# Performance work log

Measured on AMD Instinct MI355X. Metric: run time of the kernel, lower is better.

Reference implementation:

```python
import jax, jax.numpy as jnp
import numpy as np

WIN = (6, 6, 6)
HEADS = 4
DIM = 96
SPATIAL = (48, 48, 48)


def _window_partition(x, ws):
    # x: (b, d, h, w, c) -> (num_windows*b, wd*wh*ww, c)
    b, d, h, w, c = x.shape
    wd, wh, ww = ws
    x = x.reshape(b, d // wd, wd, h // wh, wh, w // ww, ww, c)
    x = x.transpose(0, 1, 3, 5, 2, 4, 6, 7)
    return x.reshape(-1, wd * wh * ww, c)


def _window_reverse(win, ws, b, d, h, w, c):
    wd, wh, ww = ws
    x = win.reshape(b, d // wd, h // wh, w // ww, wd, wh, ww, c)
    x = x.transpose(0, 1, 4, 2, 5, 3, 6, 7)
    return x.reshape(b, d, h, w, c)


def _rel_index(ws):
    # static numpy computation of relative-position index table, (n, n) int
    wd, wh, ww = ws
    coords = np.stack(np.meshgrid(np.arange(wd), np.arange(wh), np.arange(ww), indexing='ij'))
    cf = coords.reshape(3, -1)
    rc = (cf[:, :, None] - cf[:, None, :]).transpose(1, 2, 0).astype(np.int64)
    rc[..., 0] += wd - 1
    rc[..., 1] += wh - 1
    rc[..., 2] += ww - 1
    rc[..., 0] *= (2 * wh - 1) * (2 * ww - 1)
    rc[..., 1] *= (2 * ww - 1)
    return rc.sum(-1)


def _shift_mask(d, h, w, ws, ss):
    # static numpy mask, (nW, n, n) float32 with 0 / -100
    wd, wh, ww = ws
    sd, sh, sw = ss
    m = np.zeros((1, d, h, w, 1), np.float32)
    cnt = 0
    for dsl in (slice(0, -wd), slice(-wd, -sd), slice(-sd, None)):
        for hsl in (slice(0, -wh), slice(-wh, -sh), slice(-sh, None)):
            for wsl in (slice(0, -ww), slice(-ww, -sw), slice(-sw, None)):
                m[:, dsl, hsl, wsl, :] = cnt
                cnt += 1
    mw = m.reshape(1, d // wd, wd, h // wh, wh, w // ww, ww, 1)
    mw = mw.transpose(0, 1, 3, 5, 2, 4, 6, 7).reshape(-1, wd * wh * ww)
    am = mw[:, None, :] - mw[:, :, None]
    return np.where(am != 0, np.float32(-100.0), np.float32(0.0))


def _conv1x1(x, W, b):
    # 1x1x1 Conv3d == channel matmul; x: (b,c,d,h,w), W: (out,in)
    return jnp.einsum('bcdhw,oc->bodhw', x, W) + b[None, :, None, None, None]


def setup_inputs() -> dict:
    key = jax.random.key(0)
    ks = jax.random.split(key, 12)
    shp = (1, DIM) + SPATIAL
    table_size = (2 * WIN[0] - 1) * (2 * WIN[1] - 1) * (2 * WIN[2] - 1)
    s = 1.0 / np.sqrt(DIM)
    return {
        'q_in': jax.random.normal(ks[0], shp, jnp.float32),
        'k_in': jax.random.normal(ks[1], shp, jnp.float32),
        'v_in': jax.random.normal(ks[2], shp, jnp.float32),
        'Wq': jax.random.normal(ks[3], (DIM, DIM), jnp.float32) * s,
        'bq': jnp.zeros((DIM,), jnp.float32),
        'Wk': jax.random.normal(ks[4], (DIM, DIM), jnp.float32) * s,
        'bk': jnp.zeros((DIM,), jnp.float32),
        'Wv': jax.random.normal(ks[5], (DIM, DIM), jnp.float32) * s,
        'bv': jnp.zeros((DIM,), jnp.float32),
        'Wp': jax.random.normal(ks[6], (DIM, DIM), jnp.float32) * s,
        'bp': jnp.zeros((DIM,), jnp.float32),
        'rel_table': jax.random.normal(ks[7], (table_size, HEADS), jnp.float32) * 0.02,
        'use_shift': 1,
    }


def reference(q_in, k_in, v_in, Wq, bq, Wk, bk, Wv, bv, Wp, bp, rel_table, use_shift):
    b, c, d, h, w = q_in.shape
    wd, wh, ww = WIN
    hd = DIM // HEADS
    scale = hd ** -0.5
    shift = bool(use_shift)
    ss = (wd // 2, wh // 2, ww // 2) if shift else (0, 0, 0)

    q = _conv1x1(q_in, Wq, bq)
    k = _conv1x1(k_in, Wk, bk)
    v = _conv1x1(v_in, Wv, bv)
    # d,h,w divisible by window -> no padding needed
    if shift:
        q = jnp.roll(q, (-ss[0], -ss[1], -ss[2]), axis=(2, 3, 4))
        k = jnp.roll(k, (-ss[0], -ss[1], -ss[2]), axis=(2, 3, 4))
        v = jnp.roll(v, (-ss[0], -ss[1], -ss[2]), axis=(2, 3, 4))

    qw = _window_partition(q.transpose(0, 2, 3, 4, 1), WIN)
    kw = _window_partition(k.transpose(0, 2, 3, 4, 1), WIN)
    vw = _window_partition(v.transpose(0, 2, 3, 4, 1), WIN)
    nw, n, _ = qw.shape
    qw = qw.reshape(nw, n, HEADS, hd).transpose(0, 2, 1, 3)
    kw = kw.reshape(nw, n, HEADS, hd).transpose(0, 2, 1, 3)
    vw = vw.reshape(nw, n, HEADS, hd).transpose(0, 2, 1, 3)

    attn = jnp.einsum('whnd,whmd->whnm', qw * scale, kw)  # (nw, H, n, n)
    idx = _rel_index(WIN)
    bias = rel_table[idx.reshape(-1)].reshape(n, n, HEADS).transpose(2, 0, 1)
    attn = attn + bias[None]
    if shift:
        mask = jnp.asarray(_shift_mask(d, h, w, WIN, ss))  # (nW, n, n)
        nW = mask.shape[0]
        attn = attn.reshape(b, nW, HEADS, n, n) + mask[None, :, None]
        attn = attn.reshape(nw, HEADS, n, n)
    attn = jax.nn.softmax(attn, axis=-1)
    out = jnp.einsum('whnm,whmd->whnd', attn, vw)
    out = out.transpose(0, 2, 1, 3).reshape(nw, n, c)
    out = _window_reverse(out, WIN, b, d, h, w, c)
    if shift:
        out = jnp.roll(out, ss, axis=(1, 2, 3))
    out = out.transpose(0, 4, 1, 2, 3)
    out = _conv1x1(out, Wp, bp)
    return out
```

## Files before the change

### kernel.cpp

```cpp
#include <hip/hip_runtime.h>
#include <hip/hip_bf16.h>


#define CH    96
#define DS    48
#define NVOX  (48*48*48)
#define WSZ   6
#define NWIN  512
#define NTOK  216
#define NTOKP 224
#define NHEADS 4
#define HD    24
#define XSTR  100
#define VSTR  228
#define PGRID (NVOX / 128)
#define CEXP  8.0f

typedef __attribute__((ext_vector_type(4))) float  f32x4;
typedef __attribute__((ext_vector_type(4))) short  s16x4;
typedef __attribute__((ext_vector_type(8))) short  s16x8;
typedef __attribute__((ext_vector_type(8))) _Float16 f16x8;

static __device__ inline short f2b(float f) {
    union { float f; unsigned u; } v; v.f = f;
    unsigned r = v.u + 0x7FFF + ((v.u >> 16) & 1);
    return (short)(r >> 16);
}
static __device__ inline float bf2f(short s) {
    union { unsigned u; float f; } v;
    v.u = ((unsigned)(unsigned short)s) << 16;
    return v.f;
}
static __device__ inline unsigned pack_f16(float a, float b) {
    unsigned short ua = __builtin_bit_cast(unsigned short, (_Float16)a);
    unsigned short ub = __builtin_bit_cast(unsigned short, (_Float16)b);
    return (unsigned)ua | ((unsigned)ub << 16);
}

__global__ __launch_bounds__(256) void wconv_kernel(
    const float* __restrict__ W0, const float* __restrict__ W1,
    const float* __restrict__ W2, const float* __restrict__ W3,
    short* __restrict__ Wf)
{
    int idx = blockIdx.x * 256 + threadIdx.x;
    int m = idx / 9216;
    int r = idx - m * 9216;
    const float* W = (m == 0) ? W0 : ((m == 1) ? W1 : ((m == 2) ? W2 : W3));
    Wf[idx] = __builtin_bit_cast(short, (_Float16)W[r]);
}

__global__ __launch_bounds__(256) void eb_kernel(
    const float* __restrict__ rel_table, float* __restrict__ EB)
{
    int idx = blockIdx.x * 256 + threadIdx.x;
    int head = idx / (8 * NTOKP * NTOKP);
    int rem = idx - head * 8 * NTOKP * NTOKP;
    int ty = rem / (NTOKP * NTOKP);
    int rem2 = rem - ty * NTOKP * NTOKP;
    int i = rem2 / NTOKP;
    int j = rem2 - (rem2 / NTOKP) * NTOKP;
    float val = 0.f;
    if (i < NTOK && j < NTOK) {
        int tdi = i / 36, thi = (i / 6) % 6, twi = i % 6;
        int tdj = j / 36, thj = (j / 6) % 6, twj = j % 6;
        bool m = ((ty & 1) && ((tdi < 3) != (tdj < 3))) ||
                 ((ty & 2) && ((thi < 3) != (thj < 3))) ||
                 ((ty & 4) && ((twi < 3) != (twj < 3)));
        int ridx = ((tdi - tdj + 5) * 11 + (thi - thj + 5)) * 11 + (twi - twj + 5);
        float b = rel_table[ridx * NHEADS + head];
        val = m ? 0.f : __expf(b - CEXP);
    }
    EB[idx] = val;
}

__global__ __launch_bounds__(256) void proj_mfma_kernel(
    const float* __restrict__ x0, const float* __restrict__ x1, const float* __restrict__ x2,
    const short* __restrict__ Wf,
    const float* __restrict__ b0, const float* __restrict__ b1, const float* __restrict__ b2,
    const int* __restrict__ use_shift,
    short* __restrict__ d0, short* __restrict__ d1, short* __restrict__ d2,
    float scale0)
{
    __shared__ short Xs[128 * XSTR];

    int tid = threadIdx.x;
    int which = blockIdx.x / PGRID;
    int bx = blockIdx.x - which * PGRID;
    int v0 = bx * 128;

    const float* x    = (which == 0) ? x0 : ((which == 1) ? x1 : x2);
    const float* bias = (which == 0) ? b0 : ((which == 1) ? b1 : b2);
    short*       dst  = (which == 0) ? d0 : ((which == 1) ? d1 : d2);
    const short* Wfp  = Wf + which * 9216;
    float scale = (which == 0) ? scale0 : 1.0f;

    {
        int vox = tid & 127;
        int v = v0 + vox;
        int d = v / (DS * DS);
        int rem = v - d * DS * DS;
        int h = rem / DS;
        int w = rem - h * DS;
        int s = (use_shift[0] != 0) ? 3 : 0;
        int sd = d + s; if (sd >= DS) sd -= DS;
        int s_h = h + s; if (s_h >= DS) s_h -= DS;
        int s_w = w + s; if (s_w >= DS) s_w -= DS;
        int src = (sd * DS + s_h) * DS + s_w;
        for (int e = tid; e < 128 * 48; e += 256) {
            int kp = e >> 7;
            float xa = x[(2 * kp) * NVOX + src];
            float xb = x[(2 * kp + 1) * NVOX + src];
            *(unsigned*)&Xs[vox * XSTR + 2 * kp] = pack_f16(xa, xb);
        }
    }
    __syncthreads();

    const int wid = tid >> 6;
    const int lane = tid & 63;
    const int g = lane >> 4;
    const int c = lane & 15;
    const int mrow = wid * 32;

    const f32x4 zero4 = {0.f, 0.f, 0.f, 0.f};
    f32x4 acc[2][6];
#pragma unroll
    for (int i = 0; i < 2; i++)
#pragma unroll
        for (int j = 0; j < 6; j++) acc[i][j] = zero4;

#pragma unroll
    for (int kt = 0; kt < 3; kt++) {
        const short* pa0 = &Xs[(mrow + c) * XSTR + kt * 32 + g * 8];
        s16x4 a0l = *(const s16x4*)pa0;
        s16x4 a0h = *(const s16x4*)(pa0 + 4);
        f16x8 a0 = __builtin_bit_cast(f16x8,
            __builtin_shufflevector(a0l, a0h, 0, 1, 2, 3, 4, 5, 6, 7));
        const short* pa1 = &Xs[(mrow + 16 + c) * XSTR + kt * 32 + g * 8];
        s16x4 a1l = *(const s16x4*)pa1;
        s16x4 a1h = *(const s16x4*)(pa1 + 4);
        f16x8 a1 = __builtin_bit_cast(f16x8,
            __builtin_shufflevector(a1l, a1h, 0, 1, 2, 3, 4, 5, 6, 7));
#pragma unroll
        for (int nt = 0; nt < 6; nt++) {
            f16x8 bb = __builtin_bit_cast(f16x8,
                *(const s16x8*)&Wfp[(nt * 16 + c) * CH + kt * 32 + g * 8]);
            acc[0][nt] = __builtin_amdgcn_mfma_f32_16x16x32_f16(a0, bb, acc[0][nt], 0, 0, 0);
            acc[1][nt] = __builtin_amdgcn_mfma_f32_16x16x32_f16(a1, bb, acc[1][nt], 0, 0, 0);
        }
    }

    float bs[6];
#pragma unroll
    for (int nt = 0; nt < 6; nt++) bs[nt] = bias[nt * 16 + c];

    __syncthreads();

#pragma unroll
    for (int mtile = 0; mtile < 2; mtile++)
#pragma unroll
        for (int nt = 0; nt < 6; nt++)
#pragma unroll
            for (int r = 0; r < 4; r++) {
                int vox = mrow + mtile * 16 + g * 4 + r;
                int oc = nt * 16 + c;
                Xs[vox * XSTR + oc] = f2b((acc[mtile][nt][r] + bs[nt]) * scale);
            }
    __syncthreads();

    for (int e = tid; e < 512; e += 256) {
        int vox = e >> 2, q = e & 3;
        int v = v0 + vox;
        int d = v / (DS * DS);
        int rem = v - d * DS * DS;
        int h = rem / DS;
        int w = rem - h * DS;
        int widx = (d / WSZ) * 64 + (h / WSZ) * 8 + (w / WSZ);
        int tok  = (d % WSZ) * 36 + (h % WSZ) * WSZ + (w % WSZ);
        short* dp = dst + ((size_t)(widx * NHEADS + q) * NTOK + tok) * HD;
        const short* sp = &Xs[vox * XSTR + q * 24];
        s16x4 a0 = *(const s16x4*)(sp);
        s16x4 a1 = *(const s16x4*)(sp + 4);
        s16x4 a2 = *(const s16x4*)(sp + 8);
        s16x4 a3 = *(const s16x4*)(sp + 12);
        s16x4 a4 = *(const s16x4*)(sp + 16);
        s16x4 a5 = *(const s16x4*)(sp + 20);
        *(s16x8*)(dp)      = __builtin_shufflevector(a0, a1, 0, 1, 2, 3, 4, 5, 6, 7);
        *(s16x8*)(dp + 8)  = __builtin_shufflevector(a2, a3, 0, 1, 2, 3, 4, 5, 6, 7);
        *(s16x8*)(dp + 16) = __builtin_shufflevector(a4, a5, 0, 1, 2, 3, 4, 5, 6, 7);
    }
}

__global__ __launch_bounds__(256) void attn_mfma_kernel(
    const short* __restrict__ qw, const short* __restrict__ kw,
    const short* __restrict__ vw, const float* __restrict__ EB,
    const int* __restrict__ use_shift, short* __restrict__ aw)
{
    __shared__ short Ks[NTOK * 36];
    __shared__ short Vt[32 * VSTR];
    __shared__ short PO[4][576];

    int widx = blockIdx.x >> 2;
    int head = blockIdx.x & 3;
    int tid = threadIdx.x;
    bool shift = (use_shift[0] != 0);
    int wd = widx >> 6, wh = (widx >> 3) & 7, ww = widx & 7;
    int ty = shift ? ((wd == 7 ? 1 : 0) | (wh == 7 ? 2 : 0) | (ww == 7 ? 4 : 0)) : 0;

    {
        int* z2 = (int*)Ks; int* z3 = (int*)Vt;
        for (int i = tid; i < NTOK * 18; i += 256) z2[i] = 0;
        for (int i = tid; i < 16 * VSTR; i += 256)
            z3[i] = (i >= 12 * VSTR && i < (25 * VSTR) / 2) ? 0x3F803F80 : 0;
    }
    __syncthreads();

    const size_t hbase = (size_t)(widx * NHEADS + head) * NTOK * HD;

    for (int e = tid; e < NTOK * 3; e += 256) {
        int t = e / 3, ch = e - t * 3;
        const short* kp = kw + hbase + t * 24 + ch * 8;
        s16x8 k8 = *(const s16x8*)kp;
        *(s16x4*)&Ks[t * 36 + ch * 8]     = __builtin_shufflevector(k8, k8, 0, 1, 2, 3);
        *(s16x4*)&Ks[t * 36 + ch * 8 + 4] = __builtin_shufflevector(k8, k8, 4, 5, 6, 7);
        s16x8 v8 = *(const s16x8*)(vw + hbase + t * 24 + ch * 8);
#pragma unroll
        for (int j = 0; j < 8; j++) Vt[(ch * 8 + j) * VSTR + t] = v8[j];
    }
    __syncthreads();

    const int wid = tid >> 6;
    const int lane = tid & 63;
    const int g = lane >> 4;
    const int c = lane & 15;

    const f32x4 zero4 = {0.f, 0.f, 0.f, 0.f};
    short* myPs = &PO[wid][0];
    const float* EBt = EB + (size_t)(head * 8 + ty) * NTOKP * NTOKP;

    for (int mt = wid; mt < 14; mt += 4) {
        int m0 = mt * 16;
        s16x8 aq = {0, 0, 0, 0, 0, 0, 0, 0};
        int qtok = m0 + c;
        if (g < 3 && qtok < NTOK)
            aq = *(const s16x8*)(qw + hbase + (size_t)qtok * HD + g * 8);
        f32x4 sreg[14];
#pragma unroll
        for (int t = 0; t < 14; t++) {
            int krow = (t < 13) ? (t * 16 + c) : (208 + (c & 7));
            const short* p = &Ks[krow * 36 + g * 8];
            s16x4 lo = *(const s16x4*)p;
            s16x4 hi = *(const s16x4*)(p + 4);
            s16x8 bk = __builtin_shufflevector(lo, hi, 0, 1, 2, 3, 4, 5, 6, 7);
            sreg[t] = __builtin_amdgcn_mfma_f32_16x16x32_bf16(aq, bk, zero4, 0, 0, 0);
        }
        const float* ebr[4];
#pragma unroll
        for (int r = 0; r < 4; r++)
            ebr[r] = EBt + (size_t)(m0 + g * 4 + r) * NTOKP + c;
#pragma unroll
        for (int t = 0; t < 14; t++)
#pragma unroll
            for (int r = 0; r < 4; r++)
                sreg[t][r] = __expf(sreg[t][r]) * ebr[r][t * 16];

        f32x4 o0 = zero4, o1 = zero4;
#pragma unroll
        for (int kt = 0; kt < 7; kt++) {
#pragma unroll
            for (int tt = 0; tt < 2; tt++) {
                int t = kt * 2 + tt;
#pragma unroll
                for (int r = 0; r < 4; r++)
                    myPs[(g * 4 + r) * 36 + tt * 16 + c] = f2b(sreg[t][r]);
            }
            const short* p = &myPs[c * 36 + g * 8];
            s16x4 lo = *(const s16x4*)p;
            s16x4 hi = *(const s16x4*)(p + 4);
            s16x8 ap = __builtin_shufflevector(lo, hi, 0, 1, 2, 3, 4, 5, 6, 7);
            const short* pv0 = &Vt[c * VSTR + kt * 32 + g * 8];
            s16x4 v0l = *(const s16x4*)pv0;
            s16x4 v0h = *(const s16x4*)(pv0 + 4);
            s16x8 bv0 = __builtin_shufflevector(v0l, v0h, 0, 1, 2, 3, 4, 5, 6, 7);
            const short* pv1 = &Vt[(16 + c) * VSTR + kt * 32 + g * 8];
            s16x4 v1l = *(const s16x4*)pv1;
            s16x4 v1h = *(const s16x4*)(pv1 + 4);
            s16x8 bv1 = __builtin_shufflevector(v1l, v1h, 0, 1, 2, 3, 4, 5, 6, 7);
            o0 = __builtin_amdgcn_mfma_f32_16x16x32_bf16(ap, bv0, o0, 0, 0, 0);
            o1 = __builtin_amdgcn_mfma_f32_16x16x32_bf16(ap, bv1, o1, 0, 0, 0);
        }

#pragma unroll
        for (int r = 0; r < 4; r++) {
            float sm = __shfl(o1[r], (lane & 48) + 8);
            float ri = 1.f / sm;
            int row = g * 4 + r;
            myPs[row * 24 + c] = f2b(o0[r] * ri);
            if (c < 8) myPs[row * 24 + 16 + c] = f2b(o1[r] * ri);
        }
        int nrow = NTOK - m0; if (nrow > 16) nrow = 16;
        int nsh = nrow * 24;
        short* dstw = aw + hbase + (size_t)m0 * HD;
        for (int j = lane; j * 8 < nsh; j += 64)
            *(s16x8*)(dstw + j * 8) = *(const s16x8*)(myPs + j * 8);
    }
}

__global__ __launch_bounds__(256) void out_proj_mfma_kernel(
    const short* __restrict__ aw, const short* __restrict__ Wfp,
    const float* __restrict__ bp, const int* __restrict__ use_shift,
    float* __restrict__ out)
{
    __shared__ short Xs[128 * XSTR];

    int tid = threadIdx.x;
    int v0 = blockIdx.x * 128;

    for (int e = tid; e < 512; e += 256) {
        int vox = e >> 2, hq = e & 3;
        int v = v0 + vox;
        int d = v / (DS * DS);
        int rem = v - d * DS * DS;
        int h = rem / DS;
        int w = rem - h * DS;
        int s = (use_shift[0] != 0) ? 3 : 0;
        int sd = d - s; if (sd < 0) sd += DS;
        int s_h = h - s; if (s_h < 0) s_h += DS;
        int s_w = w - s; if (s_w < 0) s_w += DS;
        int widx = (sd / WSZ) * 64 + (s_h / WSZ) * 8 + (s_w / WSZ);
        int tok  = (sd % WSZ) * 36 + (s_h % WSZ) * WSZ + (s_w % WSZ);
        const short* sp = aw + ((size_t)(widx * NHEADS + hq) * NTOK + tok) * HD;
#pragma unroll
        for (int j3 = 0; j3 < 3; j3++) {
            s16x8 a = *(const s16x8*)(sp + 8 * j3);
#pragma unroll
            for (int p = 0; p < 4; p++)
                *(unsigned*)&Xs[vox * XSTR + hq * 24 + 8 * j3 + 2 * p] =
                    pack_f16(bf2f(a[2 * p]), bf2f(a[2 * p + 1]));
        }
    }
    __syncthreads();

    const int wid = tid >> 6;
    const int lane = tid & 63;
    const int g = lane >> 4;
    const int c = lane & 15;

    const f32x4 zero4 = {0.f, 0.f, 0.f, 0.f};
    f32x4 acc[2][6];
#pragma unroll
    for (int i = 0; i < 2; i++)
#pragma unroll
        for (int j = 0; j < 6; j++) acc[i][j] = zero4;

#pragma unroll
    for (int kt = 0; kt < 3; kt++) {
        f16x8 bfr[2];
#pragma unroll
        for (int mi = 0; mi < 2; mi++) {
            const short* pb = &Xs[((2 * wid + mi) * 16 + c) * XSTR + kt * 32 + g * 8];
            s16x4 bl = *(const s16x4*)pb;
            s16x4 bh = *(const s16x4*)(pb + 4);
            bfr[mi] = __builtin_bit_cast(f16x8,
                __builtin_shufflevector(bl, bh, 0, 1, 2, 3, 4, 5, 6, 7));
        }
#pragma unroll
        for (int nt = 0; nt < 6; nt++) {
            f16x8 af = __builtin_bit_cast(f16x8,
                *(const s16x8*)&Wfp[(nt * 16 + c) * CH + kt * 32 + g * 8]);
            acc[0][nt] = __builtin_amdgcn_mfma_f32_16x16x32_f16(af, bfr[0], acc[0][nt], 0, 0, 0);
            acc[1][nt] = __builtin_amdgcn_mfma_f32_16x16x32_f16(af, bfr[1], acc[1][nt], 0, 0, 0);
        }
    }

#pragma unroll
    for (int nt = 0; nt < 6; nt++)
#pragma unroll
        for (int r = 0; r < 4; r++) {
            int oc = nt * 16 + g * 4 + r;
            float bb = bp[oc];
#pragma unroll
            for (int mi = 0; mi < 2; mi++) {
                int vox = v0 + (2 * wid + mi) * 16 + c;
                out[(size_t)oc * NVOX + vox] = acc[mi][nt][r] + bb;
            }
        }
}

extern "C" void kernel_launch(void* const* d_in, const int* in_sizes, int n_in,
                              void* d_out, int out_size, void* d_ws, size_t ws_size,
                              hipStream_t stream)
{
    const float* q_in = (const float*)d_in[0];
    const float* k_in = (const float*)d_in[1];
    const float* v_in = (const float*)d_in[2];
    const float* Wq   = (const float*)d_in[3];
    const float* bq   = (const float*)d_in[4];
    const float* Wk   = (const float*)d_in[5];
    const float* bk   = (const float*)d_in[6];
    const float* Wv   = (const float*)d_in[7];
    const float* bv   = (const float*)d_in[8];
    const float* Wp   = (const float*)d_in[9];
    const float* bp   = (const float*)d_in[10];
    const float* rel_table = (const float*)d_in[11];
    const int*   use_shift = (const int*)d_in[12];

    const size_t NELEM = (size_t)NWIN * NTOK * CH;
    short* qw = (short*)d_ws;
    short* kw = qw + NELEM;
    short* vw = kw + NELEM;
    short* aw = vw + NELEM;
    short* Wf = aw + NELEM;
    float* EB = (float*)(Wf + 4 * 9216);

    const float scale = 0.20412414523193154f;

    wconv_kernel<<<144, 256, 0, stream>>>(Wq, Wk, Wv, Wp, Wf);
    eb_kernel<<<NHEADS * 8 * NTOKP * NTOKP / 256, 256, 0, stream>>>(rel_table, EB);
    proj_mfma_kernel<<<3 * PGRID, 256, 0, stream>>>(
        q_in, k_in, v_in, Wf, bq, bk, bv, use_shift, qw, kw, vw, scale);
    attn_mfma_kernel<<<NWIN * NHEADS, 256, 0, stream>>>(qw, kw, vw, EB, use_shift, aw);
    out_proj_mfma_kernel<<<PGRID, 256, 0, stream>>>(aw, Wf + 3 * 9216, bp, use_shift, (float*)d_out);
}
```

Measured before the change: 279.4 us.

## Store exp-bias table as bf16 in tile-major layout and drop block syncs in projections

The precomputed exp(bias)*mask table becomes bf16 and is reordered so each lane loads its 14 column-tile values for a row with two 16-byte loads, where before it made many strided fp32 loads. This halves the table's footprint and traffic in the attention kernel, at the cost of bf16 rounding of the bias factor. Separately, the input and output projection kernels now assign each wave the same voxel rows it later computes on, which lets the __syncthreads barriers be removed. That ordering depends on intra-wave visibility of LDS writes.

```diff
diff --git a/kernel.cpp b/kernel.cpp
--- a/kernel.cpp
+++ b/kernel.cpp
@@ -50,7 +50,7 @@
 }
 
 __global__ __launch_bounds__(256) void eb_kernel(
-    const float* __restrict__ rel_table, float* __restrict__ EB)
+    const float* __restrict__ rel_table, short* __restrict__ EBb)
 {
     int idx = blockIdx.x * 256 + threadIdx.x;
     int head = idx / (8 * NTOKP * NTOKP);
@@ -70,7 +70,8 @@
         float b = rel_table[ridx * NHEADS + head];
         val = m ? 0.f : __expf(b - CEXP);
     }
-    EB[idx] = val;
+    int t = j >> 4, c = j & 15;
+    EBb[(((size_t)(head * 8 + ty) * NTOKP + i) * 16 + c) * 16 + t] = f2b(val);
 }
 
 __global__ __launch_bounds__(256) void proj_mfma_kernel(
@@ -94,8 +95,12 @@
     const short* Wfp  = Wf + which * 9216;
     float scale = (which == 0) ? scale0 : 1.0f;
 
+    const int wid = tid >> 6;
+    const int lane = tid & 63;
+    const int mrow = wid * 32;
+
     {
-        int vox = tid & 127;
+        int vox = mrow + (lane & 31);
         int v = v0 + vox;
         int d = v / (DS * DS);
         int rem = v - d * DS * DS;
@@ -106,20 +111,18 @@
         int s_h = h + s; if (s_h >= DS) s_h -= DS;
         int s_w = w + s; if (s_w >= DS) s_w -= DS;
         int src = (sd * DS + s_h) * DS + s_w;
-        for (int e = tid; e < 128 * 48; e += 256) {
-            int kp = e >> 7;
-            float xa = x[(2 * kp) * NVOX + src];
-            float xb = x[(2 * kp + 1) * NVOX + src];
-            *(unsigned*)&Xs[vox * XSTR + 2 * kp] = pack_f16(xa, xb);
-        }
-    }
-    __syncthreads();
-
-    const int wid = tid >> 6;
-    const int lane = tid & 63;
+        int half = lane >> 5;
+#pragma unroll 4
+        for (int kq = 0; kq < 24; kq++) {
+            int chp = kq * 2 + half;
+            float xa = x[(2 * chp) * NVOX + src];
+            float xb = x[(2 * chp + 1) * NVOX + src];
+            *(unsigned*)&Xs[vox * XSTR + 2 * chp] = pack_f16(xa, xb);
+        }
+    }
+
     const int g = lane >> 4;
     const int c = lane & 15;
-    const int mrow = wid * 32;
 
     const f32x4 zero4 = {0.f, 0.f, 0.f, 0.f};
     f32x4 acc[2][6];
@@ -153,8 +156,6 @@
 #pragma unroll
     for (int nt = 0; nt < 6; nt++) bs[nt] = bias[nt * 16 + c];
 
-    __syncthreads();
-
 #pragma unroll
     for (int mtile = 0; mtile < 2; mtile++)
 #pragma unroll
@@ -165,10 +166,11 @@
                 int oc = nt * 16 + c;
                 Xs[vox * XSTR + oc] = f2b((acc[mtile][nt][r] + bs[nt]) * scale);
             }
-    __syncthreads();
-
-    for (int e = tid; e < 512; e += 256) {
-        int vox = e >> 2, q = e & 3;
+
+#pragma unroll
+    for (int it = 0; it < 2; it++) {
+        int u = lane + it * 64;
+        int vox = mrow + (u >> 2), q = u & 3;
         int v = v0 + vox;
         int d = v / (DS * DS);
         int rem = v - d * DS * DS;
@@ -192,7 +194,7 @@
 
 __global__ __launch_bounds__(256) void attn_mfma_kernel(
     const short* __restrict__ qw, const short* __restrict__ kw,
-    const short* __restrict__ vw, const float* __restrict__ EB,
+    const short* __restrict__ vw, const short* __restrict__ EBb,
     const int* __restrict__ use_shift, short* __restrict__ aw)
 {
     __shared__ short Ks[NTOK * 36];
@@ -235,7 +237,7 @@
 
     const f32x4 zero4 = {0.f, 0.f, 0.f, 0.f};
     short* myPs = &PO[wid][0];
-    const float* EBt = EB + (size_t)(head * 8 + ty) * NTOKP * NTOKP;
+    const short* ebB = EBb + (size_t)(head * 8 + ty) * NTOKP * 256;
 
     for (int mt = wid; mt < 14; mt += 4) {
         int m0 = mt * 16;
@@ -253,15 +255,17 @@
             s16x8 bk = __builtin_shufflevector(lo, hi, 0, 1, 2, 3, 4, 5, 6, 7);
             sreg[t] = __builtin_amdgcn_mfma_f32_16x16x32_bf16(aq, bk, zero4, 0, 0, 0);
         }
-        const float* ebr[4];
-#pragma unroll
-        for (int r = 0; r < 4; r++)
-            ebr[r] = EBt + (size_t)(m0 + g * 4 + r) * NTOKP + c;
-#pragma unroll
-        for (int t = 0; t < 14; t++)
-#pragma unroll
-            for (int r = 0; r < 4; r++)
-                sreg[t][r] = __expf(sreg[t][r]) * ebr[r][t * 16];
+#pragma unroll
+        for (int r = 0; r < 4; r++) {
+            const short* er = ebB + ((size_t)(m0 + g * 4 + r) * 16 + c) * 16;
+            s16x8 e0 = *(const s16x8*)er;
+            s16x8 e1 = *(const s16x8*)(er + 8);
+#pragma unroll
+            for (int t = 0; t < 14; t++) {
+                float eb = bf2f(t < 8 ? e0[t] : e1[t - 8]);
+                sreg[t][r] = __expf(sreg[t][r]) * eb;
+            }
+        }
 
         f32x4 o0 = zero4, o1 = zero4;
 #pragma unroll
@@ -314,9 +318,14 @@
 
     int tid = threadIdx.x;
     int v0 = blockIdx.x * 128;
-
-    for (int e = tid; e < 512; e += 256) {
-        int vox = e >> 2, hq = e & 3;
+    const int wid = tid >> 6;
+    const int lane = tid & 63;
+    const int mrow = wid * 32;
+
+#pragma unroll
+    for (int it = 0; it < 2; it++) {
+        int u = lane + it * 64;
+        int vox = mrow + (u >> 2), hq = u & 3;
         int v = v0 + vox;
         int d = v / (DS * DS);
         int rem = v - d * DS * DS;
@@ -338,10 +347,7 @@
                     pack_f16(bf2f(a[2 * p]), bf2f(a[2 * p + 1]));
         }
     }
-    __syncthreads();
-
-    const int wid = tid >> 6;
-    const int lane = tid & 63;
+
     const int g = lane >> 4;
     const int c = lane & 15;
 
@@ -357,7 +363,7 @@
         f16x8 bfr[2];
 #pragma unroll
         for (int mi = 0; mi < 2; mi++) {
-            const short* pb = &Xs[((2 * wid + mi) * 16 + c) * XSTR + kt * 32 + g * 8];
+            const short* pb = &Xs[(mrow + mi * 16 + c) * XSTR + kt * 32 + g * 8];
             s16x4 bl = *(const s16x4*)pb;
             s16x4 bh = *(const s16x4*)(pb + 4);
             bfr[mi] = __builtin_bit_cast(f16x8,
@@ -380,7 +386,7 @@
             float bb = bp[oc];
 #pragma unroll
             for (int mi = 0; mi < 2; mi++) {
-                int vox = v0 + (2 * wid + mi) * 16 + c;
+                int vox = v0 + mrow + mi * 16 + c;
                 out[(size_t)oc * NVOX + vox] = acc[mi][nt][r] + bb;
             }
         }
@@ -410,14 +416,14 @@
     short* vw = kw + NELEM;
     short* aw = vw + NELEM;
     short* Wf = aw + NELEM;
-    float* EB = (float*)(Wf + 4 * 9216);
+    short* EBb = Wf + 4 * 9216;
 
     const float scale = 0.20412414523193154f;
 
     wconv_kernel<<<144, 256, 0, stream>>>(Wq, Wk, Wv, Wp, Wf);
-    eb_kernel<<<NHEADS * 8 * NTOKP * NTOKP / 256, 256, 0, stream>>>(rel_table, EB);
+    eb_kernel<<<NHEADS * 8 * NTOKP * NTOKP / 256, 256, 0, stream>>>(rel_table, EBb);
     proj_mfma_kernel<<<3 * PGRID, 256, 0, stream>>>(
         q_in, k_in, v_in, Wf, bq, bk, bv, use_shift, qw, kw, vw, scale);
-    attn_mfma_kernel<<<NWIN * NHEADS, 256, 0, stream>>>(qw, kw, vw, EB, use_shift, aw);
+    attn_mfma_kernel<<<NWIN * NHEADS, 256, 0, stream>>>(qw, kw, vw, EBb, use_shift, aw);
     out_proj_mfma_kernel<<<PGRID, 256, 0, stream>>>(aw, Wf + 3 * 9216, bp, use_shift, (float*)d_out);
 }
```

Measured after the change: 287.7 us. 1.03x slower.
